# Performance work log

Measured on AMD Instinct MI355X. Metric: run time of the kernel, lower is better.

Reference implementation:

```python
import jax, jax.numpy as jnp
import numpy as np

N_HEAD = 16

def setup_inputs() -> dict:
    key = jax.random.key(0)
    ks = jax.random.split(key, 9)
    H = 2048
    def w(k, shape, scale=0.02):
        return jax.random.normal(k, shape, dtype=jnp.float32) * scale
    return {
        'h':  jax.random.normal(ks[0], (4, 2048, H), dtype=jnp.float32),
        'Wq': w(ks[1], (H, H)), 'bq': w(ks[2], (H,)),
        'Wk': w(ks[3], (H, H)), 'bk': w(ks[4], (H,)),
        'Wv': w(ks[5], (H, H)), 'bv': w(ks[6], (H,)),
        'Wo': w(ks[7], (H, H)), 'bo': w(ks[8], (H,)),
    }

def reference(h, Wq, bq, Wk, bk, Wv, bv, Wo, bo):
    B, S, H = h.shape
    nh = N_HEAD
    hd = H // nh
    # QKV projections (torch Linear: x @ W.T + b)
    q = (h @ Wq.T + bq).reshape(B, S, nh, hd)
    k = (h @ Wk.T + bk).reshape(B, S, nh, hd)
    v = (h @ Wv.T + bv).reshape(B, S, nh, hd)
    scale = 1.0 / jnp.sqrt(jnp.float32(hd))
    # causal attention scores [B, nh, S, S]
    scores = jnp.einsum('bqhd,bkhd->bhqk', q, k) * scale
    causal = jnp.tril(jnp.ones((S, S), dtype=bool))
    scores = jnp.where(causal, scores, jnp.finfo(scores.dtype).min)
    attn = jax.nn.softmax(scores, axis=-1)
    o = jnp.einsum('bhqk,bkhd->bqhd', attn, v).reshape(B, S, H)
    return o @ Wo.T + bo
```

## Files before the change

### kernel.cpp

```cpp
#include <hip/hip_runtime.h>
#include <hip/hip_bf16.h>
#include <math.h>


using bf16x8 = __attribute__((ext_vector_type(8))) __bf16;
using f32x4  = __attribute__((ext_vector_type(4))) float;
using s16x8  = __attribute__((ext_vector_type(8))) short;

#define MFMA16(a, b, c) __builtin_amdgcn_mfma_f32_16x16x32_bf16((a), (b), (c), 0, 0, 0)

__device__ __forceinline__ unsigned short f2bf(float f) {
  unsigned u = __float_as_uint(f);
  u += 0x7FFFu + ((u >> 16) & 1u);
  return (unsigned short)(u >> 16);
}

__device__ __forceinline__ void gload16(const void* g, void* l) {
  __builtin_amdgcn_global_load_lds((const __attribute__((address_space(1))) void*)g,
                                   (__attribute__((address_space(3))) void*)l,
                                   16, 0, 0);
}

__global__ void cvt_kernel(const float* __restrict__ in, unsigned short* __restrict__ out, int n4) {
  int i = blockIdx.x * 256 + threadIdx.x;
  if (i >= n4) return;
  float4 v = ((const float4*)in)[i];
  ushort4 o;
  o.x = f2bf(v.x); o.y = f2bf(v.y); o.z = f2bf(v.z); o.w = f2bf(v.w);
  ((ushort4*)out)[i] = o;
}

__global__ void cvtW_kernel(const float* __restrict__ s0, const float* __restrict__ s1,
                            const float* __restrict__ s2, const float* __restrict__ s3,
                            unsigned short* __restrict__ dqkv, unsigned short* __restrict__ dwo) {
  int i = blockIdx.x * 256 + threadIdx.x;
  int which = i >> 20;
  const float* s = (which == 0) ? s0 : (which == 1) ? s1 : (which == 2) ? s2 : s3;
  unsigned short* d = (which < 3) ? dqkv + which * 4194304 : dwo;
  int j = i & 1048575;
  float4 v = ((const float4*)s)[j];
  ushort4 o;
  o.x = f2bf(v.x); o.y = f2bf(v.y); o.z = f2bf(v.z); o.w = f2bf(v.w);
  ((ushort4*)d)[j] = o;
}


#define GEMM_PRE()                                                             \
  const int tid = threadIdx.x;                                                 \
  const int wave = tid >> 6, lane = tid & 63;                                  \
  const int lo = lane & 15, hi = lane >> 4;                                    \
  const int wr = wave >> 2, wc = wave & 3;                                     \
  const int r4 = lane >> 2, s4 = lane & 3;                                     \
  const int scol = ((s4 ^ ((r4 >> 1) & 3)) << 3);                              \
  const unsigned short* aBase[2]; const unsigned short* bBase[2];              \
  _Pragma("unroll")                                                            \
  for (int j = 0; j < 2; ++j) {                                                \
    aBase[j] = A + (size_t)(m0 + (wave * 2 + j) * 16 + r4) * 2048 + scol;      \
    bBase[j] = W + (size_t)(n0 + (wave * 2 + j) * 16 + r4) * 2048 + scol;      \
  }                                                                            \
  f32x4 acc[8][4] = {};

#define STAGEA(BUF, KH, KOFF)                                                  \
  do {                                                                         \
    _Pragma("unroll")                                                          \
    for (int j = 0; j < 2; ++j)                                                \
      gload16(aBase[j] + (KOFF), &lA[BUF][KH][(wave * 2 + j) * 512]);          \
  } while (0)

#define STAGEB(BUF, KH, KOFF)                                                  \
  do {                                                                         \
    _Pragma("unroll")                                                          \
    for (int j = 0; j < 2; ++j)                                                \
      gload16(bBase[j] + (KOFF), &lB[BUF][KH][(wave * 2 + j) * 512]);          \
  } while (0)

#define LDA4_(dst, MH, BUF, KH)                                                \
  do {                                                                         \
    _Pragma("unroll")                                                          \
    for (int im = 0; im < 4; ++im)                                             \
      dst[im] = *(const bf16x8*)&lA[BUF][KH][(wr * 128 + (MH)*64 + im * 16 + lo) * 32 + \
                                             ((hi ^ ((lo >> 1) & 3)) << 3)];   \
  } while (0)

#define LDB4_(dst, BUF, KH)                                                    \
  do {                                                                         \
    _Pragma("unroll")                                                          \
    for (int ni = 0; ni < 4; ++ni)                                             \
      dst[ni] = *(const bf16x8*)&lB[BUF][KH][(wc * 64 + ni * 16 + lo) * 32 +   \
                                             ((hi ^ ((lo >> 1) & 3)) << 3)];   \
  } while (0)

#define MF16(MH, aF, bF)                                                       \
  do {                                                                         \
    __builtin_amdgcn_s_setprio(1);                                             \
    _Pragma("unroll")                                                          \
    for (int im = 0; im < 4; ++im)                                             \
      _Pragma("unroll")                                                        \
      for (int ni = 0; ni < 4; ++ni)                                           \
        acc[(MH)*4 + im][ni] = MFMA16(aF[im], bF[ni], acc[(MH)*4 + im][ni]);   \
    __builtin_amdgcn_s_setprio(0);                                             \
  } while (0)

#define BAR __builtin_amdgcn_s_barrier()
#define VMC(N) asm volatile("s_waitcnt vmcnt(" #N ")" ::: "memory")

#define TILE64(B, BX, C1, C2, VN)                                              \
  do {                                                                         \
    bf16x8 aF[4], aG[4], bF[4];                                                \
    LDA4_(aF, 0, B, 0); LDB4_(bF, B, 0);                                       \
    if (C1) STAGEA(BX, 1, kbase + 96);                                         \
    BAR; MF16(0, aF, bF); BAR;                                                 \
    LDA4_(aG, 1, B, 0);                                                        \
    if (C1) STAGEB(BX, 1, kbase + 96);                                         \
    BAR; MF16(1, aG, bF); BAR;                                                 \
    LDA4_(aF, 0, B, 1); LDB4_(bF, B, 1);                                       \
    if (C2) STAGEA(B, 0, kbase + 128);                                         \
    BAR; MF16(0, aF, bF); BAR;                                                 \
    LDA4_(aG, 1, B, 1);                                                        \
    if (C2) STAGEB(B, 0, kbase + 128);                                         \
    BAR; MF16(1, aG, bF); VMC(VN); BAR;                                        \
    kbase += 64;                                                               \
  } while (0)

#define GEMM_MAIN()                                                            \
  int kbase = 0;                                                               \
  STAGEA(0, 0, 0); STAGEB(0, 0, 0);                                            \
  STAGEA(0, 1, 32); STAGEB(0, 1, 32);                                          \
  STAGEA(1, 0, 64); STAGEB(1, 0, 64);                                          \
  VMC(4); BAR;                                                                 \
  for (int u = 0; u < 14; ++u) {                                               \
    TILE64(0, 1, true, true, 4); TILE64(1, 0, true, true, 4);                  \
  }                                                                            \
  TILE64(0, 1, true, true, 4);                                                 \
  TILE64(1, 0, true, true, 4);                                                 \
  TILE64(0, 1, true, false, 0);                                                \
  TILE64(1, 0, false, false, 0);

__global__ __launch_bounds__(512, 2)
void gemm_qkv(const unsigned short* __restrict__ A,
              const unsigned short* __restrict__ W,
              const float* __restrict__ bq, const float* __restrict__ bk,
              const float* __restrict__ bv,
              unsigned short* __restrict__ Q, unsigned short* __restrict__ Kq,
              unsigned short* __restrict__ V) {
  __shared__ unsigned short lA[2][2][256 * 32];
  __shared__ unsigned short lB[2][2][256 * 32];
  const int bid = blockIdx.x;
  const int sid = (bid & 7) * 96 + (bid >> 3);
  const int bm = sid / 24, bn = sid % 24;
  const int m0 = bm * 256, n0 = bn * 256;
  GEMM_PRE();
  GEMM_MAIN();

  const int which = n0 >> 11;
  const float* bias = (which == 0) ? bq : (which == 1) ? bk : bv;
  unsigned short* dst = (which == 0) ? Q : (which == 1) ? Kq : V;
#pragma unroll
  for (int mi = 0; mi < 8; mi++)
#pragma unroll
    for (int ni = 0; ni < 4; ni++) {
      int n_g = n0 + wc * 64 + ni * 16 + lo;
      int n2 = n_g & 2047;
      int head = n2 >> 7, d = n2 & 127;
      float bb = bias[n2];
#pragma unroll
      for (int i = 0; i < 4; i++) {
        int m = m0 + wr * 128 + mi * 16 + hi * 4 + i;
        int b = m >> 11, s = m & 2047;
        dst[(((size_t)b * 16 + head) * 2048 + s) * 128 + d] = f2bf(acc[mi][ni][i] + bb);
      }
    }
}

__global__ __launch_bounds__(512, 2)
void gemm_out(const unsigned short* __restrict__ A,
              const unsigned short* __restrict__ W,
              const float* __restrict__ bo, float* __restrict__ out) {
  __shared__ unsigned short lA[2][2][256 * 32];
  __shared__ unsigned short lB[2][2][256 * 32];
  const int bid = blockIdx.x;
  const int sid = (bid & 7) * 32 + (bid >> 3);
  const int bm = sid >> 3, bn = sid & 7;
  const int m0 = bm * 256, n0 = bn * 256;
  GEMM_PRE();
  GEMM_MAIN();

#pragma unroll
  for (int mi = 0; mi < 8; mi++)
#pragma unroll
    for (int ni = 0; ni < 4; ni++) {
      int n_g = n0 + wc * 64 + ni * 16 + lo;
      float bb = bo[n_g];
#pragma unroll
      for (int i = 0; i < 4; i++) {
        int m = m0 + wr * 128 + mi * 16 + hi * 4 + i;
        out[(size_t)m * 2048 + n_g] = acc[mi][ni][i] + bb;
      }
    }
}

__global__ __launch_bounds__(256, 2)
void attn_kernel(const unsigned short* __restrict__ Qb,
                 const unsigned short* __restrict__ Kb,
                 const unsigned short* __restrict__ Vb,
                 unsigned short* __restrict__ Ob) {
  __shared__ unsigned short lK[2][64 * 128];
  __shared__ unsigned short lVt[144 * 72];
  __shared__ unsigned short lP[4][32 * 72];

  const int tid = threadIdx.x;
  const int wave = tid >> 6, lane = tid & 63;
  const int lo = lane & 15, hi = lane >> 4;
  const int bh = blockIdx.x & 63;
  const int qt = 15 - (blockIdx.x >> 6);
  const int q0 = qt * 128 + wave * 32;
  const size_t base = (size_t)bh * 2048 * 128;
  const float SCL = 0.08838834764831845f * 1.4426950408889634f;
  const float THR = 11.5416f;

#pragma unroll
  for (int x = tid; x < 1024; x += 256)
    lVt[(128 + (x >> 6)) * 72 + (x & 63)] = 0x3F80;

  bf16x8 aq[2][4];
#pragma unroll
  for (int mi = 0; mi < 2; mi++)
#pragma unroll
    for (int dk = 0; dk < 4; dk++)
      aq[mi][dk] = *(const bf16x8*)&Qb[base + (size_t)(q0 + mi * 16 + lo) * 128 + dk * 32 + hi * 8];

  f32x4 acc[2][9] = {};
  float mrun[2][4];
#pragma unroll
  for (int a = 0; a < 2; a++)
#pragma unroll
    for (int b = 0; b < 4; b++) mrun[a][b] = -INFINITY;

  const int ktn = qt * 2 + 2;
  const int qmax_w = q0 + 31;
  const int rr = tid & 31, c0v = (tid >> 5) * 8;

#define STAGEK(KT2, BUF)                                                       \
  do {                                                                         \
    _Pragma("unroll")                                                          \
    for (int j = 0; j < 4; j++) {                                              \
      int lrow = j * 16 + wave * 4 + hi;                                       \
      int srccol = (lo * 16) ^ ((lrow & 7) << 4);                              \
      gload16(Kb + base + (size_t)((KT2) * 64 + lrow) * 128 + (srccol >> 1),   \
              &lK[BUF][(j * 16 + wave * 4) * 128]);                            \
    }                                                                          \
  } while (0)

  STAGEK(0, 0);

  for (int kt = 0; kt < ktn; kt++) {
    const unsigned short* vp0 = Vb + base + (size_t)(kt * 64 + 2 * rr) * 128 + c0v;
    s16x8 v00 = *(const s16x8*)vp0;
    s16x8 v01 = *(const s16x8*)(vp0 + 128);
    s16x8 v10 = *(const s16x8*)(vp0 + 64);
    s16x8 v11 = *(const s16x8*)(vp0 + 192);
    if (kt + 1 < ktn) { STAGEK(kt + 1, (kt + 1) & 1); VMC(8); }
    else { VMC(4); }
    BAR;

    const bool docomp = (kt * 64 <= qmax_w);
    if (docomp) {
      const unsigned short* lKc = &lK[kt & 1][0];
      f32x4 sc[2][4] = {};
#pragma unroll
      for (int ni = 0; ni < 4; ni++)
#pragma unroll
        for (int dk = 0; dk < 4; dk++) {
          int row = ni * 16 + lo;
          int col = (dk * 32 + hi * 8) ^ ((row & 7) << 3);
          bf16x8 bk_ = *(const bf16x8*)&lKc[row * 128 + col];
          sc[0][ni] = MFMA16(aq[0][dk], bk_, sc[0][ni]);
          sc[1][ni] = MFMA16(aq[1][dk], bk_, sc[1][ni]);
        }
      float tm[2][4];
      bool cond = true;
#pragma unroll
      for (int mi = 0; mi < 2; mi++)
#pragma unroll
        for (int i = 0; i < 4; i++) {
          int qrow = q0 + mi * 16 + hi * 4 + i;
          float mx = -INFINITY;
#pragma unroll
          for (int ni = 0; ni < 4; ni++) {
            int kc = kt * 64 + ni * 16 + lo;
            float s = sc[mi][ni][i] * SCL;
            if (kc > qrow) s = -INFINITY;
            sc[mi][ni][i] = s;
            mx = fmaxf(mx, s);
          }
          tm[mi][i] = mx;
          cond = cond && (mx <= mrun[mi][i] + THR);
        }
      if (!__all((int)cond)) {
#pragma unroll
        for (int mi = 0; mi < 2; mi++)
#pragma unroll
          for (int i = 0; i < 4; i++) {
            float mt = tm[mi][i];
            mt = fmaxf(mt, __shfl_xor(mt, 1));
            mt = fmaxf(mt, __shfl_xor(mt, 2));
            mt = fmaxf(mt, __shfl_xor(mt, 4));
            mt = fmaxf(mt, __shfl_xor(mt, 8));
            float mo = mrun[mi][i];
            float mn = fmaxf(mo, mt);
            float alpha = exp2f(mo - mn);
            mrun[mi][i] = mn;
#pragma unroll
            for (int ni = 0; ni < 9; ni++) acc[mi][ni][i] *= alpha;
          }
      }
      unsigned short* lPw = &lP[wave][0];
#pragma unroll
      for (int mi = 0; mi < 2; mi++)
#pragma unroll
        for (int i = 0; i < 4; i++) {
          float m = mrun[mi][i];
          int prow = mi * 16 + hi * 4 + i;
#pragma unroll
          for (int ni = 0; ni < 4; ni++)
            lPw[prow * 72 + ni * 16 + lo] = f2bf(exp2f(sc[mi][ni][i] - m));
        }
    }

    if (kt + 1 < ktn) VMC(4); else VMC(0);
#pragma unroll
    for (int j = 0; j < 8; j++) {
      *(ushort2*)&lVt[(c0v + j) * 72 + 2 * rr] =
          make_ushort2((unsigned short)v00[j], (unsigned short)v01[j]);
      *(ushort2*)&lVt[(c0v + 64 + j) * 72 + 2 * rr] =
          make_ushort2((unsigned short)v10[j], (unsigned short)v11[j]);
    }
    asm volatile("s_waitcnt lgkmcnt(0)" ::: "memory");
    BAR;

    if (docomp) {
      unsigned short* lPw = &lP[wave][0];
      bf16x8 ap[2][2];
#pragma unroll
      for (int mi = 0; mi < 2; mi++)
#pragma unroll
        for (int k2 = 0; k2 < 2; k2++)
          ap[mi][k2] = *(const bf16x8*)&lPw[(mi * 16 + lo) * 72 + k2 * 32 + hi * 8];
#pragma unroll
      for (int ni = 0; ni < 9; ni++)
#pragma unroll
        for (int k2 = 0; k2 < 2; k2++) {
          bf16x8 bv_ = *(const bf16x8*)&lVt[(ni * 16 + lo) * 72 + k2 * 32 + hi * 8];
          acc[0][ni] = MFMA16(ap[0][k2], bv_, acc[0][ni]);
          acc[1][ni] = MFMA16(ap[1][k2], bv_, acc[1][ni]);
        }
    }
  }

  const int b = bh >> 4, hh = bh & 15;
#pragma unroll
  for (int mi = 0; mi < 2; mi++)
#pragma unroll
    for (int i = 0; i < 4; i++) {
      float inv = 1.0f / acc[mi][8][i];
      int s = q0 + mi * 16 + hi * 4 + i;
      size_t rowbase = ((size_t)b * 2048 + s) * 2048 + hh * 128 + lo;
#pragma unroll
      for (int ni = 0; ni < 8; ni++)
        Ob[rowbase + ni * 16] = f2bf(acc[mi][ni][i] * inv);
    }
}

extern "C" void kernel_launch(void* const* d_in, const int* in_sizes, int n_in,
                              void* d_out, int out_size, void* d_ws, size_t ws_size,
                              hipStream_t stream) {
  const float* h  = (const float*)d_in[0];
  const float* Wq = (const float*)d_in[1];
  const float* bq = (const float*)d_in[2];
  const float* Wk = (const float*)d_in[3];
  const float* bk = (const float*)d_in[4];
  const float* Wv = (const float*)d_in[5];
  const float* bv = (const float*)d_in[6];
  const float* Wo = (const float*)d_in[7];
  const float* bo = (const float*)d_in[8];
  float* out = (float*)d_out;

  char* ws = (char*)d_ws;
  unsigned short* h_bf  = (unsigned short*)(ws + 0);
  unsigned short* Qb    = (unsigned short*)(ws + 33554432);
  unsigned short* Kb    = (unsigned short*)(ws + 67108864);
  unsigned short* Vb    = (unsigned short*)(ws + 100663296);
  unsigned short* Wqkv  = (unsigned short*)(ws + 134217728);
  unsigned short* Wo_bf = (unsigned short*)(ws + 159383552);
  unsigned short* Ob    = h_bf;

  cvt_kernel<<<16384, 256, 0, stream>>>(h, h_bf, 4194304);
  cvtW_kernel<<<16384, 256, 0, stream>>>(Wq, Wk, Wv, Wo, Wqkv, Wo_bf);

  gemm_qkv<<<dim3(768), dim3(512), 0, stream>>>(h_bf, Wqkv, bq, bk, bv, Qb, Kb, Vb);

  attn_kernel<<<dim3(1024), dim3(256), 0, stream>>>(Qb, Kb, Vb, Ob);

  gemm_out<<<dim3(256), dim3(512), 0, stream>>>(Ob, Wo_bf, bo, out);
}
```

Before: 450.6 us.

## Restructure GEMM LDS pipeline to four 32-wide K stages and raise MFMA priority in attention

The GEMM staging changes from a double buffer of 64-wide K tiles (two 32-wide halves each) to a four-slot ring of 32-wide K slices. Global-to-LDS prefetch runs three slices ahead, and the load pointers advance incrementally instead of being computed from a running offset. In the attention kernel, the V register loads are now waited on before the barrier instead of after softmax, and setprio raises wave priority around the QK and PV MFMA loops. The deeper prefetch aims to hide more memory latency; the trade-off is more barriers per unit of K and an earlier vmcnt wait in attention that can stall.

```diff
diff --git a/kernel.cpp b/kernel.cpp
--- a/kernel.cpp
+++ b/kernel.cpp
@@ -52,42 +52,35 @@
   const int wr = wave >> 2, wc = wave & 3;                                     \
   const int r4 = lane >> 2, s4 = lane & 3;                                     \
   const int scol = ((s4 ^ ((r4 >> 1) & 3)) << 3);                              \
-  const unsigned short* aBase[2]; const unsigned short* bBase[2];              \
+  const unsigned short* aS[2]; const unsigned short* bS[2];                    \
   _Pragma("unroll")                                                            \
   for (int j = 0; j < 2; ++j) {                                                \
-    aBase[j] = A + (size_t)(m0 + (wave * 2 + j) * 16 + r4) * 2048 + scol;      \
-    bBase[j] = W + (size_t)(n0 + (wave * 2 + j) * 16 + r4) * 2048 + scol;      \
+    aS[j] = A + (size_t)(m0 + (wave * 2 + j) * 16 + r4) * 2048 + scol;         \
+    bS[j] = W + (size_t)(n0 + (wave * 2 + j) * 16 + r4) * 2048 + scol;         \
   }                                                                            \
   f32x4 acc[8][4] = {};
 
-#define STAGEA(BUF, KH, KOFF)                                                  \
-  do {                                                                         \
-    _Pragma("unroll")                                                          \
-    for (int j = 0; j < 2; ++j)                                                \
-      gload16(aBase[j] + (KOFF), &lA[BUF][KH][(wave * 2 + j) * 512]);          \
-  } while (0)
-
-#define STAGEB(BUF, KH, KOFF)                                                  \
-  do {                                                                         \
-    _Pragma("unroll")                                                          \
-    for (int j = 0; j < 2; ++j)                                                \
-      gload16(bBase[j] + (KOFF), &lB[BUF][KH][(wave * 2 + j) * 512]);          \
-  } while (0)
-
-#define LDA4_(dst, MH, BUF, KH)                                                \
+#define STAGE2(BUF, J)                                                         \
+  do {                                                                         \
+    gload16(aS[J], &lA[BUF][(wave * 2 + (J)) * 512]);                          \
+    gload16(bS[J], &lB[BUF][(wave * 2 + (J)) * 512]);                          \
+    aS[J] += 32; bS[J] += 32;                                                  \
+  } while (0)
+
+#define LDA4_(dst, MH, BUF)                                                    \
   do {                                                                         \
     _Pragma("unroll")                                                          \
     for (int im = 0; im < 4; ++im)                                             \
-      dst[im] = *(const bf16x8*)&lA[BUF][KH][(wr * 128 + (MH)*64 + im * 16 + lo) * 32 + \
-                                             ((hi ^ ((lo >> 1) & 3)) << 3)];   \
-  } while (0)
-
-#define LDB4_(dst, BUF, KH)                                                    \
+      dst[im] = *(const bf16x8*)&lA[BUF][(wr * 128 + (MH)*64 + im * 16 + lo) * 32 + \
+                                         ((hi ^ ((lo >> 1) & 3)) << 3)];       \
+  } while (0)
+
+#define LDB4_(dst, BUF)                                                        \
   do {                                                                         \
     _Pragma("unroll")                                                          \
     for (int ni = 0; ni < 4; ++ni)                                             \
-      dst[ni] = *(const bf16x8*)&lB[BUF][KH][(wc * 64 + ni * 16 + lo) * 32 +   \
-                                             ((hi ^ ((lo >> 1) & 3)) << 3)];   \
+      dst[ni] = *(const bf16x8*)&lB[BUF][(wc * 64 + ni * 16 + lo) * 32 +       \
+                                         ((hi ^ ((lo >> 1) & 3)) << 3)];       \
   } while (0)
 
 #define MF16(MH, aF, bF)                                                       \
@@ -104,37 +97,27 @@
 #define BAR __builtin_amdgcn_s_barrier()
 #define VMC(N) asm volatile("s_waitcnt vmcnt(" #N ")" ::: "memory")
 
-#define TILE64(B, BX, C1, C2, VN)                                              \
+#define TILE(RBUF, SBUF, COND, VN)                                             \
   do {                                                                         \
     bf16x8 aF[4], aG[4], bF[4];                                                \
-    LDA4_(aF, 0, B, 0); LDB4_(bF, B, 0);                                       \
-    if (C1) STAGEA(BX, 1, kbase + 96);                                         \
+    LDA4_(aF, 0, RBUF); LDB4_(bF, RBUF);                                       \
+    if (COND) STAGE2(SBUF, 0);                                                 \
     BAR; MF16(0, aF, bF); BAR;                                                 \
-    LDA4_(aG, 1, B, 0);                                                        \
-    if (C1) STAGEB(BX, 1, kbase + 96);                                         \
-    BAR; MF16(1, aG, bF); BAR;                                                 \
-    LDA4_(aF, 0, B, 1); LDB4_(bF, B, 1);                                       \
-    if (C2) STAGEA(B, 0, kbase + 128);                                         \
-    BAR; MF16(0, aF, bF); BAR;                                                 \
-    LDA4_(aG, 1, B, 1);                                                        \
-    if (C2) STAGEB(B, 0, kbase + 128);                                         \
+    LDA4_(aG, 1, RBUF);                                                        \
+    if (COND) STAGE2(SBUF, 1);                                                 \
     BAR; MF16(1, aG, bF); VMC(VN); BAR;                                        \
-    kbase += 64;                                                               \
   } while (0)
 
 #define GEMM_MAIN()                                                            \
-  int kbase = 0;                                                               \
-  STAGEA(0, 0, 0); STAGEB(0, 0, 0);                                            \
-  STAGEA(0, 1, 32); STAGEB(0, 1, 32);                                          \
-  STAGEA(1, 0, 64); STAGEB(1, 0, 64);                                          \
-  VMC(4); BAR;                                                                 \
-  for (int u = 0; u < 14; ++u) {                                               \
-    TILE64(0, 1, true, true, 4); TILE64(1, 0, true, true, 4);                  \
+  STAGE2(0, 0); STAGE2(0, 1); STAGE2(1, 0); STAGE2(1, 1);                      \
+  STAGE2(2, 0); STAGE2(2, 1);                                                  \
+  VMC(8); BAR;                                                                 \
+  for (int u = 0; u < 15; ++u) {                                               \
+    TILE(0, 3, true, 8); TILE(1, 0, true, 8);                                  \
+    TILE(2, 1, true, 8); TILE(3, 2, true, 8);                                  \
   }                                                                            \
-  TILE64(0, 1, true, true, 4);                                                 \
-  TILE64(1, 0, true, true, 4);                                                 \
-  TILE64(0, 1, true, false, 0);                                                \
-  TILE64(1, 0, false, false, 0);
+  TILE(0, 3, true, 8); TILE(1, 0, false, 4);                                   \
+  TILE(2, 1, false, 0); TILE(3, 2, false, 0);
 
 __global__ __launch_bounds__(512, 2)
 void gemm_qkv(const unsigned short* __restrict__ A,
@@ -143,8 +126,8 @@
               const float* __restrict__ bv,
               unsigned short* __restrict__ Q, unsigned short* __restrict__ Kq,
               unsigned short* __restrict__ V) {
-  __shared__ unsigned short lA[2][2][256 * 32];
-  __shared__ unsigned short lB[2][2][256 * 32];
+  __shared__ unsigned short lA[4][256 * 32];
+  __shared__ unsigned short lB[4][256 * 32];
   const int bid = blockIdx.x;
   const int sid = (bid & 7) * 96 + (bid >> 3);
   const int bm = sid / 24, bn = sid % 24;
@@ -176,8 +159,8 @@
 void gemm_out(const unsigned short* __restrict__ A,
               const unsigned short* __restrict__ W,
               const float* __restrict__ bo, float* __restrict__ out) {
-  __shared__ unsigned short lA[2][2][256 * 32];
-  __shared__ unsigned short lB[2][2][256 * 32];
+  __shared__ unsigned short lA[4][256 * 32];
+  __shared__ unsigned short lB[4][256 * 32];
   const int bid = blockIdx.x;
   const int sid = (bid & 7) * 32 + (bid >> 3);
   const int bm = sid >> 3, bn = sid & 7;
@@ -260,13 +243,14 @@
     s16x8 v10 = *(const s16x8*)(vp0 + 64);
     s16x8 v11 = *(const s16x8*)(vp0 + 192);
     if (kt + 1 < ktn) { STAGEK(kt + 1, (kt + 1) & 1); VMC(8); }
-    else { VMC(4); }
+    else { VMC(0); }
     BAR;
 
     const bool docomp = (kt * 64 <= qmax_w);
     if (docomp) {
       const unsigned short* lKc = &lK[kt & 1][0];
       f32x4 sc[2][4] = {};
+      __builtin_amdgcn_s_setprio(1);
 #pragma unroll
       for (int ni = 0; ni < 4; ni++)
 #pragma unroll
@@ -277,6 +261,7 @@
           sc[0][ni] = MFMA16(aq[0][dk], bk_, sc[0][ni]);
           sc[1][ni] = MFMA16(aq[1][dk], bk_, sc[1][ni]);
         }
+      __builtin_amdgcn_s_setprio(0);
       float tm[2][4];
       bool cond = true;
 #pragma unroll
@@ -327,7 +312,6 @@
         }
     }
 
-    if (kt + 1 < ktn) VMC(4); else VMC(0);
 #pragma unroll
     for (int j = 0; j < 8; j++) {
       *(ushort2*)&lVt[(c0v + j) * 72 + 2 * rr] =
@@ -346,6 +330,7 @@
 #pragma unroll
         for (int k2 = 0; k2 < 2; k2++)
           ap[mi][k2] = *(const bf16x8*)&lPw[(mi * 16 + lo) * 72 + k2 * 32 + hi * 8];
+      __builtin_amdgcn_s_setprio(1);
 #pragma unroll
       for (int ni = 0; ni < 9; ni++)
 #pragma unroll
@@ -354,6 +339,7 @@
           acc[0][ni] = MFMA16(ap[0][k2], bv_, acc[0][ni]);
           acc[1][ni] = MFMA16(ap[1][k2], bv_, acc[1][ni]);
         }
+      __builtin_amdgcn_s_setprio(0);
     }
   }
 
```

After: 431.8 us. -4.2%, faster.
